# Optimization experiments

Measured on AMD Instinct MI355X. Metric: run time of the kernel, lower is better.

## Reference

```python
import jax, jax.numpy as jnp
import numpy as np

N_NODES = 50000
N_EDGES = 800000
IN_DIM = 128
OUT_DIM = 64
OUT_DATA = 32


def glorot(key, shape):
    fan_in, fan_out = shape[0], shape[1]
    lim = (6.0 / (fan_in + fan_out)) ** 0.5
    return jax.random.uniform(key, shape, jnp.float32, -lim, lim)


def setup_inputs() -> dict:
    key = jax.random.key(0)
    ks = jax.random.split(key, 8)
    x = jax.random.normal(ks[0], (N_NODES, IN_DIM), jnp.float32)
    edge_index = jax.random.randint(ks[1], (2, N_EDGES), 0, N_NODES, jnp.int64)
    W1 = glorot(ks[2], (IN_DIM, OUT_DIM)); b1 = jnp.zeros((OUT_DIM,), jnp.float32)
    W2 = glorot(ks[3], (OUT_DIM, OUT_DIM)); b2 = jnp.zeros((OUT_DIM,), jnp.float32)
    Wp1 = glorot(ks[4], (OUT_DIM, OUT_DIM)); bp1 = jnp.zeros((OUT_DIM,), jnp.float32)
    Wp2 = glorot(ks[5], (OUT_DIM, OUT_DATA)); bp2 = jnp.zeros((OUT_DATA,), jnp.float32)
    return {"x": x, "edge_index": edge_index, "W1": W1, "b1": b1,
            "W2": W2, "b2": b2, "Wp1": Wp1, "bp1": bp1, "Wp2": Wp2, "bp2": bp2}


def gcn_conv(x, src, dst, W, b, num_nodes):
    # GCNConv with symmetric normalization and self-loops:
    # out = D^{-1/2} (A + I) D^{-1/2} (x W) + b
    xw = x @ W                                            # [N, F]
    deg = jnp.zeros((num_nodes,), xw.dtype).at[dst].add(1.0) + 1.0  # +1 self-loop
    dinv = jax.lax.rsqrt(deg)
    coef = dinv[src] * dinv[dst]                          # [E]
    msgs = xw[src] * coef[:, None]                        # gather + scale
    agg = jax.ops.segment_sum(msgs, dst, num_segments=num_nodes)
    agg = agg + xw * (dinv * dinv)[:, None]               # self-loop term
    return agg + b


def reference(x, edge_index, W1, b1, W2, b2, Wp1, bp1, Wp2, bp2):
    src, dst = edge_index[0], edge_index[1]
    n = x.shape[0]
    # layer 1
    h = gcn_conv(x, src, dst, W1, b1, n)
    h = jnp.tanh(h)  # dropout is identity at inference
    # layer 2
    h = gcn_conv(h, src, dst, W2, b2, n)
    embedding = h
    h = jnp.tanh(h)
    # post_mp head: Linear -> Dropout(identity) -> Linear
    h = h @ Wp1 + bp1
    logits = h @ Wp2 + bp2
    return embedding, jax.nn.log_softmax(logits, axis=1)
```

## Files before the change

kernel.cpp:

```cpp
#include <hip/hip_runtime.h>
#include <hip/hip_fp16.h>

#define N_NODES 50000
#define N_EDGES 800000
#define IN_DIM 128
#define OUT_DIM 64
#define OUT_DATA 32

#define BUCKET_SHIFT 6
#define BUCKET_SIZE 64
#define NBUCK ((N_NODES + BUCKET_SIZE - 1) / BUCKET_SIZE)
#define NBLK_BIN 128
#define BIN_THREADS 1024
#define EPB ((N_EDGES + NBLK_BIN - 1) / NBLK_BIN)
#define ELCAP 1536

#define OFF_GCNT    0u
#define OFF_GBASE   4096u
#define OFF_DEG     8192u
#define OFF_NSTART  208896u
#define OFF_PERBLK  409600u
#define OFF_EREC    811008u
#define OFF_EREC2   4012032u
#define OFF_XW      7213056u
#define OFF_XW2     13613056u
#define OFF_WC      20013056u
#define OFF_BC      20021248u

__device__ __forceinline__ bool ei_is64(const int* ei) {
    int o = 0;
#pragma unroll
    for (int k = 0; k < 16; ++k) o |= ei[2 * k + 1];
    return o == 0;
}
__device__ __forceinline__ int load_ei(const int* ei, long long flat, bool is64) {
    return is64 ? (int)(((const long long*)ei)[flat]) : ei[flat];
}

__global__ void zero_kernel(int4* __restrict__ p) {
    p[threadIdx.x] = make_int4(0, 0, 0, 0);
}

__global__ __launch_bounds__(BIN_THREADS) void hist_kernel(const int* __restrict__ ei,
                                                           int* __restrict__ gcnt,
                                                           int* __restrict__ perblk) {
    __shared__ int lh[NBUCK];
    int t = threadIdx.x;
    for (int i = t; i < NBUCK; i += BIN_THREADS) lh[i] = 0;
    __syncthreads();
    bool is64 = ei_is64(ei);
    int e0 = blockIdx.x * EPB;
    int e1 = e0 + EPB; if (e1 > N_EDGES) e1 = N_EDGES;
    for (int e = e0 + t; e < e1; e += BIN_THREADS) {
        int d = load_ei(ei, (long long)N_EDGES + e, is64);
        atomicAdd(&lh[d >> BUCKET_SHIFT], 1);
    }
    __syncthreads();
    for (int i = t; i < NBUCK; i += BIN_THREADS)
        perblk[blockIdx.x * NBUCK + i] = atomicAdd(&gcnt[i], lh[i]);
}

__global__ __launch_bounds__(1024) void scanP_kernel(
    const int* __restrict__ gcnt, int* __restrict__ gbase,
    const float* __restrict__ Wp1, const float* __restrict__ bp1,
    const float* __restrict__ Wp2, const float* __restrict__ bp2,
    float* __restrict__ Wc, float* __restrict__ bc) {
    __shared__ int tmp[1024];
    int t = threadIdx.x;
    int v = (t < NBUCK) ? gcnt[t] : 0;
    tmp[t] = v;
    __syncthreads();
    for (int o = 1; o < 1024; o <<= 1) {
        int x = tmp[t];
        if (t >= o) x += tmp[t - o];
        __syncthreads();
        tmp[t] = x;
        __syncthreads();
    }
    if (t < NBUCK) gbase[t] = tmp[t] - v;
    if (t == NBUCK - 1) gbase[NBUCK] = tmp[t];
    for (int idx = t; idx < 64 * 32; idx += 1024) {
        int r = idx >> 5, j = idx & 31;
        float s = 0.0f;
        for (int k = 0; k < 64; ++k) s += Wp1[r * 64 + k] * Wp2[k * 32 + j];
        Wc[idx] = s;
    }
    if (t < 32) {
        float s = bp2[t];
        for (int k = 0; k < 64; ++k) s += bp1[k] * Wp2[k * 32 + t];
        bc[t] = s;
    }
}

__global__ __launch_bounds__(BIN_THREADS) void scat_kernel(const int* __restrict__ ei,
                                                           const int* __restrict__ gbase,
                                                           const int* __restrict__ perblk,
                                                           int* __restrict__ erec) {
    __shared__ int lh[NBUCK];
    __shared__ int base[NBUCK];
    int t = threadIdx.x;
    for (int i = t; i < NBUCK; i += BIN_THREADS) {
        lh[i] = 0;
        base[i] = gbase[i] + perblk[blockIdx.x * NBUCK + i];
    }
    __syncthreads();
    bool is64 = ei_is64(ei);
    int e0 = blockIdx.x * EPB;
    int e1 = e0 + EPB; if (e1 > N_EDGES) e1 = N_EDGES;
    for (int e = e0 + t; e < e1; e += BIN_THREADS) {
        int s = load_ei(ei, e, is64);
        int d = load_ei(ei, (long long)N_EDGES + e, is64);
        int b = d >> BUCKET_SHIFT;
        int slot = atomicAdd(&lh[b], 1);
        erec[base[b] + slot] = s | ((d & (BUCKET_SIZE - 1)) << 16);
    }
}

__global__ __launch_bounds__(512) void sortK_kernel(const int* __restrict__ erec,
                                                    const int* __restrict__ gbase,
                                                    int* __restrict__ erec2,
                                                    int* __restrict__ nodeStart,
                                                    int* __restrict__ deg) {
    __shared__ int elist[ELCAP];
    __shared__ int lcntS[64];
    __shared__ int startS[65];
    int t = threadIdx.x;
    int ebeg = gbase[blockIdx.x], eend = gbase[blockIdx.x + 1];
    int ecnt = eend - ebeg; if (ecnt > ELCAP) ecnt = ELCAP;
    for (int i = t; i < ecnt; i += 512) elist[i] = erec[ebeg + i];
    if (t < 64) lcntS[t] = 0;
    __syncthreads();
    int rec0 = -1, rank0 = 0, rec1 = -1, rank1 = 0, rec2 = -1, rank2 = 0;
    { int i = t;        if (i < ecnt) { rec0 = elist[i]; rank0 = atomicAdd(&lcntS[rec0 >> 16], 1); } }
    { int i = t + 512;  if (i < ecnt) { rec1 = elist[i]; rank1 = atomicAdd(&lcntS[rec1 >> 16], 1); } }
    { int i = t + 1024; if (i < ecnt) { rec2 = elist[i]; rank2 = atomicAdd(&lcntS[rec2 >> 16], 1); } }
    __syncthreads();
    if (t < 64) {
        int vcnt = lcntS[t]; int sum = vcnt;
        for (int off = 1; off < 64; off <<= 1) {
            int o = __shfl_up(sum, off, 64);
            if (t >= off) sum += o;
        }
        startS[t + 1] = sum; if (t == 0) startS[0] = 0;
    }
    __syncthreads();
    if (rec0 >= 0) erec2[ebeg + startS[rec0 >> 16] + rank0] = rec0;
    if (rec1 >= 0) erec2[ebeg + startS[rec1 >> 16] + rank1] = rec1;
    if (rec2 >= 0) erec2[ebeg + startS[rec2 >> 16] + rank2] = rec2;
    if (t < 64) {
        int node = (blockIdx.x << BUCKET_SHIFT) + t;
        nodeStart[node] = ebeg + startS[t];
        deg[node] = startS[t + 1] - startS[t];
    }
}

template <int K>
__global__ __launch_bounds__(256) void gemm64_kernel(const float* __restrict__ X,
                                                     const float* __restrict__ W,
                                                     const int* __restrict__ deg,
                                                     __half* __restrict__ Yh, int N) {
    __shared__ float Wl[K * 64];
    int t = threadIdx.x;
    for (int i = t; i < K * 16; i += 256)
        reinterpret_cast<float4*>(Wl)[i] = reinterpret_cast<const float4*>(W)[i];
    __syncthreads();
    int row = blockIdx.x * 256 + t;
    if (row >= N) return;
    float acc[64];
#pragma unroll
    for (int c = 0; c < 64; ++c) acc[c] = 0.0f;
    const float4* xr = reinterpret_cast<const float4*>(X + (size_t)row * K);
    for (int k4 = 0; k4 < K / 4; ++k4) {
        float4 xv = xr[k4];
#pragma unroll
        for (int kk = 0; kk < 4; ++kk) {
            float xs = (kk == 0) ? xv.x : (kk == 1) ? xv.y : (kk == 2) ? xv.z : xv.w;
            const float4* wr = reinterpret_cast<const float4*>(&Wl[(k4 * 4 + kk) * 64]);
#pragma unroll
            for (int c4 = 0; c4 < 16; ++c4) {
                float4 wv = wr[c4];
                acc[c4 * 4 + 0] += xs * wv.x;
                acc[c4 * 4 + 1] += xs * wv.y;
                acc[c4 * 4 + 2] += xs * wv.z;
                acc[c4 * 4 + 3] += xs * wv.w;
            }
        }
    }
    float di = rsqrtf((float)deg[row] + 1.0f);
    __half2* yr = reinterpret_cast<__half2*>(Yh + (size_t)row * 64);
#pragma unroll
    for (int c2 = 0; c2 < 32; ++c2)
        yr[c2] = __floats2half2_rn(acc[2 * c2] * di, acc[2 * c2 + 1] * di);
}

__device__ __forceinline__ float gatherN(const __half* __restrict__ xwp,
                                         const int* __restrict__ er,
                                         int s0, int n, int lane) {
    float acc = 0.0f;
    int e = 0;
    for (; e + 16 <= n; e += 16) {
        int r[16];
#pragma unroll
        for (int k = 0; k < 16; ++k) r[k] = er[s0 + e + k];
        float v[16];
#pragma unroll
        for (int k = 0; k < 16; ++k) v[k] = __half2float(xwp[((r[k] & 0xFFFF) << 6) + lane]);
#pragma unroll
        for (int k = 0; k < 16; ++k) acc += v[k];
    }
    if (e + 8 <= n) {
        int r[8];
#pragma unroll
        for (int k = 0; k < 8; ++k) r[k] = er[s0 + e + k];
        float v[8];
#pragma unroll
        for (int k = 0; k < 8; ++k) v[k] = __half2float(xwp[((r[k] & 0xFFFF) << 6) + lane]);
#pragma unroll
        for (int k = 0; k < 8; ++k) acc += v[k];
        e += 8;
    }
    if (e + 4 <= n) {
        int r[4];
#pragma unroll
        for (int k = 0; k < 4; ++k) r[k] = er[s0 + e + k];
        float v[4];
#pragma unroll
        for (int k = 0; k < 4; ++k) v[k] = __half2float(xwp[((r[k] & 0xFFFF) << 6) + lane]);
#pragma unroll
        for (int k = 0; k < 4; ++k) acc += v[k];
        e += 4;
    }
    for (; e < n; ++e)
        acc += __half2float(xwp[((er[s0 + e] & 0xFFFF) << 6) + lane]);
    return acc;
}

__global__ __launch_bounds__(256) void aggA_kernel(
    const __half* __restrict__ xwp, const int* __restrict__ erec2,
    const int* __restrict__ nodeStart, const int* __restrict__ deg,
    const float* __restrict__ b1v, const float* __restrict__ W2,
    __half* __restrict__ xw2p) {
    __shared__ float W2l[64 * 64];
    __shared__ float rowS[4][64];
    int t = threadIdx.x;
    for (int i = t; i < 1024; i += 256)
        reinterpret_cast<float4*>(W2l)[i] = reinterpret_cast<const float4*>(W2)[i];
    __syncthreads();
    int node = __builtin_amdgcn_readfirstlane(blockIdx.x * 4 + (t >> 6));
    if (node >= N_NODES) return;
    int lane = t & 63, wib = t >> 6;
    int s0 = __builtin_amdgcn_readfirstlane(nodeStart[node]);
    int n  = __builtin_amdgcn_readfirstlane(deg[node]);
    float acc = gatherN(xwp, erec2, s0, n, lane);
    float selfv = __half2float(xwp[(node << 6) + lane]);
    float di = rsqrtf((float)n + 1.0f);
    float h = tanhf((acc + selfv) * di + b1v[lane]);
    rowS[wib][lane] = h;
    float o = 0.0f;
#pragma unroll
    for (int f4 = 0; f4 < 16; ++f4) {
        float4 rv = reinterpret_cast<const float4*>(&rowS[wib][0])[f4];
        o += rv.x * W2l[(f4 * 4 + 0) * 64 + lane];
        o += rv.y * W2l[(f4 * 4 + 1) * 64 + lane];
        o += rv.z * W2l[(f4 * 4 + 2) * 64 + lane];
        o += rv.w * W2l[(f4 * 4 + 3) * 64 + lane];
    }
    xw2p[(node << 6) + lane] = __float2half_rn(o * di);
}

__global__ __launch_bounds__(256) void aggB_kernel(
    const __half* __restrict__ xw2p, const int* __restrict__ erec2,
    const int* __restrict__ nodeStart, const int* __restrict__ deg,
    const float* __restrict__ b2v, const float* __restrict__ Wc,
    const float* __restrict__ bc, float* __restrict__ embOut,
    float* __restrict__ logitsOut) {
    __shared__ float Wcl[64 * 32];
    __shared__ float rowS[4][64];
    __shared__ float bcl[32];
    int t = threadIdx.x;
    for (int i = t; i < 512; i += 256)
        reinterpret_cast<float4*>(Wcl)[i] = reinterpret_cast<const float4*>(Wc)[i];
    if (t < 32) bcl[t] = bc[t];
    __syncthreads();
    int node = __builtin_amdgcn_readfirstlane(blockIdx.x * 4 + (t >> 6));
    if (node >= N_NODES) return;
    int lane = t & 63, wib = t >> 6;
    int s0 = __builtin_amdgcn_readfirstlane(nodeStart[node]);
    int n  = __builtin_amdgcn_readfirstlane(deg[node]);
    float acc = gatherN(xw2p, erec2, s0, n, lane);
    float selfv = __half2float(xw2p[(node << 6) + lane]);
    float di = rsqrtf((float)n + 1.0f);
    float v = (acc + selfv) * di + b2v[lane];
    embOut[(node << 6) + lane] = v;
    rowS[wib][lane] = tanhf(v);
    int j = lane & 31, half = lane >> 5;
    float p = half ? 0.0f : bcl[j];
#pragma unroll
    for (int f4 = 0; f4 < 8; ++f4) {
        float4 rv = reinterpret_cast<const float4*>(&rowS[wib][half * 32])[f4];
        int fb = half * 32 + f4 * 4;
        p += rv.x * Wcl[(fb + 0) * 32 + j];
        p += rv.y * Wcl[(fb + 1) * 32 + j];
        p += rv.z * Wcl[(fb + 2) * 32 + j];
        p += rv.w * Wcl[(fb + 3) * 32 + j];
    }
    p += __shfl_down(p, 32);
    float m = p;
#pragma unroll
    for (int o = 16; o > 0; o >>= 1) m = fmaxf(m, __shfl_xor(m, o, 32));
    float ex = __expf(p - m);
    float s = ex;
#pragma unroll
    for (int o = 16; o > 0; o >>= 1) s += __shfl_xor(s, o, 32);
    if (half == 0) logitsOut[node * 32 + j] = p - m - logf(s);
}

extern "C" void kernel_launch(void* const* d_in, const int* in_sizes, int n_in,
                              void* d_out, int out_size, void* d_ws, size_t ws_size,
                              hipStream_t stream) {
    const float* x   = (const float*)d_in[0];
    const int*   ei  = (const int*)d_in[1];
    const float* W1  = (const float*)d_in[2];
    const float* b1  = (const float*)d_in[3];
    const float* W2  = (const float*)d_in[4];
    const float* b2  = (const float*)d_in[5];
    const float* Wp1 = (const float*)d_in[6];
    const float* bp1 = (const float*)d_in[7];
    const float* Wp2 = (const float*)d_in[8];
    const float* bp2 = (const float*)d_in[9];

    char* ws = (char*)d_ws;
    int*    gcnt   = (int*)(ws + OFF_GCNT);
    int*    gbase  = (int*)(ws + OFF_GBASE);
    int*    deg    = (int*)(ws + OFF_DEG);
    int*    nstart = (int*)(ws + OFF_NSTART);
    int*    perblk = (int*)(ws + OFF_PERBLK);
    int*    erec   = (int*)(ws + OFF_EREC);
    int*    erec2  = (int*)(ws + OFF_EREC2);
    __half* xwp    = (__half*)(ws + OFF_XW);
    __half* xw2p   = (__half*)(ws + OFF_XW2);
    float*  Wc     = (float*)(ws + OFF_WC);
    float*  bc     = (float*)(ws + OFF_BC);

    float* emb_out    = (float*)d_out;
    float* logits_out = (float*)d_out + (size_t)N_NODES * 64;

    zero_kernel<<<1, 256, 0, stream>>>((int4*)(ws + OFF_GCNT));
    hist_kernel<<<NBLK_BIN, BIN_THREADS, 0, stream>>>(ei, gcnt, perblk);
    scanP_kernel<<<1, 1024, 0, stream>>>(gcnt, gbase, Wp1, bp1, Wp2, bp2, Wc, bc);
    scat_kernel<<<NBLK_BIN, BIN_THREADS, 0, stream>>>(ei, gbase, perblk, erec);
    sortK_kernel<<<NBUCK, 512, 0, stream>>>(erec, gbase, erec2, nstart, deg);

    gemm64_kernel<IN_DIM><<<(N_NODES + 255) / 256, 256, 0, stream>>>(x, W1, deg, xwp, N_NODES);
    aggA_kernel<<<(N_NODES + 3) / 4, 256, 0, stream>>>(xwp, erec2, nstart, deg, b1, W2, xw2p);
    aggB_kernel<<<(N_NODES + 3) / 4, 256, 0, stream>>>(xw2p, erec2, nstart, deg, b2, Wc, bc, emb_out, logits_out);
}
```

Before: 141.7 us.

## Fuse per-bucket sort into layer-1 aggregation, compute degrees in histogram

The separate sortK kernel is removed. Its per-bucket counting sort now runs inside aggA, which works on one 64-node bucket per block and reads neighbour lists from shared memory. Degrees come from global atomics in the histogram kernel, so zero_kernel is widened to clear the degree array. The GEMM now computes two rows per thread. This removes a launch and a global round trip for the sorted edges, but adds global atomics and makes aggA run fewer, heavier blocks, each wave looping over 16 nodes, which may hurt load balance and occupancy.

```diff
diff --git a/kernel.cpp b/kernel.cpp
--- a/kernel.cpp
+++ b/kernel.cpp
@@ -38,12 +38,14 @@
 }
 
 __global__ void zero_kernel(int4* __restrict__ p) {
-    p[threadIdx.x] = make_int4(0, 0, 0, 0);
+    int i = blockIdx.x * 256 + threadIdx.x;
+    if (i < 13056) p[i] = make_int4(0, 0, 0, 0);
 }
 
 __global__ __launch_bounds__(BIN_THREADS) void hist_kernel(const int* __restrict__ ei,
                                                            int* __restrict__ gcnt,
-                                                           int* __restrict__ perblk) {
+                                                           int* __restrict__ perblk,
+                                                           int* __restrict__ deg) {
     __shared__ int lh[NBUCK];
     int t = threadIdx.x;
     for (int i = t; i < NBUCK; i += BIN_THREADS) lh[i] = 0;
@@ -54,6 +56,7 @@
     for (int e = e0 + t; e < e1; e += BIN_THREADS) {
         int d = load_ei(ei, (long long)N_EDGES + e, is64);
         atomicAdd(&lh[d >> BUCKET_SHIFT], 1);
+        atomicAdd(&deg[d], 1);
     }
     __syncthreads();
     for (int i = t; i < NBUCK; i += BIN_THREADS)
@@ -116,44 +119,6 @@
     }
 }
 
-__global__ __launch_bounds__(512) void sortK_kernel(const int* __restrict__ erec,
-                                                    const int* __restrict__ gbase,
-                                                    int* __restrict__ erec2,
-                                                    int* __restrict__ nodeStart,
-                                                    int* __restrict__ deg) {
-    __shared__ int elist[ELCAP];
-    __shared__ int lcntS[64];
-    __shared__ int startS[65];
-    int t = threadIdx.x;
-    int ebeg = gbase[blockIdx.x], eend = gbase[blockIdx.x + 1];
-    int ecnt = eend - ebeg; if (ecnt > ELCAP) ecnt = ELCAP;
-    for (int i = t; i < ecnt; i += 512) elist[i] = erec[ebeg + i];
-    if (t < 64) lcntS[t] = 0;
-    __syncthreads();
-    int rec0 = -1, rank0 = 0, rec1 = -1, rank1 = 0, rec2 = -1, rank2 = 0;
-    { int i = t;        if (i < ecnt) { rec0 = elist[i]; rank0 = atomicAdd(&lcntS[rec0 >> 16], 1); } }
-    { int i = t + 512;  if (i < ecnt) { rec1 = elist[i]; rank1 = atomicAdd(&lcntS[rec1 >> 16], 1); } }
-    { int i = t + 1024; if (i < ecnt) { rec2 = elist[i]; rank2 = atomicAdd(&lcntS[rec2 >> 16], 1); } }
-    __syncthreads();
-    if (t < 64) {
-        int vcnt = lcntS[t]; int sum = vcnt;
-        for (int off = 1; off < 64; off <<= 1) {
-            int o = __shfl_up(sum, off, 64);
-            if (t >= off) sum += o;
-        }
-        startS[t + 1] = sum; if (t == 0) startS[0] = 0;
-    }
-    __syncthreads();
-    if (rec0 >= 0) erec2[ebeg + startS[rec0 >> 16] + rank0] = rec0;
-    if (rec1 >= 0) erec2[ebeg + startS[rec1 >> 16] + rank1] = rec1;
-    if (rec2 >= 0) erec2[ebeg + startS[rec2 >> 16] + rank2] = rec2;
-    if (t < 64) {
-        int node = (blockIdx.x << BUCKET_SHIFT) + t;
-        nodeStart[node] = ebeg + startS[t];
-        deg[node] = startS[t + 1] - startS[t];
-    }
-}
-
 template <int K>
 __global__ __launch_bounds__(256) void gemm64_kernel(const float* __restrict__ X,
                                                      const float* __restrict__ W,
@@ -164,33 +129,138 @@
     for (int i = t; i < K * 16; i += 256)
         reinterpret_cast<float4*>(Wl)[i] = reinterpret_cast<const float4*>(W)[i];
     __syncthreads();
-    int row = blockIdx.x * 256 + t;
-    if (row >= N) return;
-    float acc[64];
-#pragma unroll
-    for (int c = 0; c < 64; ++c) acc[c] = 0.0f;
-    const float4* xr = reinterpret_cast<const float4*>(X + (size_t)row * K);
+    int row0 = blockIdx.x * 512 + t;
+    int row1 = row0 + 256;
+    if (row0 >= N) return;
+    bool p1 = row1 < N;
+    float acc0[64], acc1[64];
+#pragma unroll
+    for (int c = 0; c < 64; ++c) { acc0[c] = 0.0f; acc1[c] = 0.0f; }
+    const float4* xr0 = reinterpret_cast<const float4*>(X + (size_t)row0 * K);
+    const float4* xr1 = reinterpret_cast<const float4*>(X + (size_t)(p1 ? row1 : row0) * K);
     for (int k4 = 0; k4 < K / 4; ++k4) {
-        float4 xv = xr[k4];
+        float4 xv0 = xr0[k4];
+        float4 xv1 = xr1[k4];
 #pragma unroll
         for (int kk = 0; kk < 4; ++kk) {
-            float xs = (kk == 0) ? xv.x : (kk == 1) ? xv.y : (kk == 2) ? xv.z : xv.w;
+            float xs0 = (kk == 0) ? xv0.x : (kk == 1) ? xv0.y : (kk == 2) ? xv0.z : xv0.w;
+            float xs1 = (kk == 0) ? xv1.x : (kk == 1) ? xv1.y : (kk == 2) ? xv1.z : xv1.w;
             const float4* wr = reinterpret_cast<const float4*>(&Wl[(k4 * 4 + kk) * 64]);
 #pragma unroll
             for (int c4 = 0; c4 < 16; ++c4) {
                 float4 wv = wr[c4];
-                acc[c4 * 4 + 0] += xs * wv.x;
-                acc[c4 * 4 + 1] += xs * wv.y;
-                acc[c4 * 4 + 2] += xs * wv.z;
-                acc[c4 * 4 + 3] += xs * wv.w;
+                acc0[c4 * 4 + 0] += xs0 * wv.x; acc1[c4 * 4 + 0] += xs1 * wv.x;
+                acc0[c4 * 4 + 1] += xs0 * wv.y; acc1[c4 * 4 + 1] += xs1 * wv.y;
+                acc0[c4 * 4 + 2] += xs0 * wv.z; acc1[c4 * 4 + 2] += xs1 * wv.z;
+                acc0[c4 * 4 + 3] += xs0 * wv.w; acc1[c4 * 4 + 3] += xs1 * wv.w;
             }
         }
     }
-    float di = rsqrtf((float)deg[row] + 1.0f);
-    __half2* yr = reinterpret_cast<__half2*>(Yh + (size_t)row * 64);
+    float di0 = rsqrtf((float)deg[row0] + 1.0f);
+    __half2* yr0 = reinterpret_cast<__half2*>(Yh + (size_t)row0 * 64);
 #pragma unroll
     for (int c2 = 0; c2 < 32; ++c2)
-        yr[c2] = __floats2half2_rn(acc[2 * c2] * di, acc[2 * c2 + 1] * di);
+        yr0[c2] = __floats2half2_rn(acc0[2 * c2] * di0, acc0[2 * c2 + 1] * di0);
+    if (p1) {
+        float di1 = rsqrtf((float)deg[row1] + 1.0f);
+        __half2* yr1 = reinterpret_cast<__half2*>(Yh + (size_t)row1 * 64);
+#pragma unroll
+        for (int c2 = 0; c2 < 32; ++c2)
+            yr1[c2] = __floats2half2_rn(acc1[2 * c2] * di1, acc1[2 * c2 + 1] * di1);
+    }
+}
+
+__global__ __launch_bounds__(256) void aggA_kernel(
+    const __half* __restrict__ xwp, const int* __restrict__ erec,
+    const int* __restrict__ gbase, const float* __restrict__ b1v,
+    const float* __restrict__ W2, int* __restrict__ erec2,
+    int* __restrict__ nodeStart, __half* __restrict__ xw2p) {
+    __shared__ int elist[ELCAP];
+    __shared__ int elist2[ELCAP];
+    __shared__ float W2l[64 * 64];
+    __shared__ float rowS[4][64];
+    __shared__ int lcntS[64];
+    __shared__ int startS[65];
+    int t = threadIdx.x;
+    for (int i = t; i < 1024; i += 256)
+        reinterpret_cast<float4*>(W2l)[i] = reinterpret_cast<const float4*>(W2)[i];
+    int ebeg = gbase[blockIdx.x], eend = gbase[blockIdx.x + 1];
+    int ecnt = eend - ebeg; if (ecnt > ELCAP) ecnt = ELCAP;
+    for (int i = t; i < ecnt; i += 256) elist[i] = erec[ebeg + i];
+    if (t < 64) lcntS[t] = 0;
+    __syncthreads();
+    int rec[6], rank[6];
+#pragma unroll
+    for (int c = 0; c < 6; ++c) {
+        int i = t + c * 256;
+        rec[c] = -1; rank[c] = 0;
+        if (i < ecnt) { rec[c] = elist[i]; rank[c] = atomicAdd(&lcntS[rec[c] >> 16], 1); }
+    }
+    __syncthreads();
+    if (t < 64) {
+        int v = lcntS[t]; int sum = v;
+        for (int off = 1; off < 64; off <<= 1) {
+            int o = __shfl_up(sum, off, 64);
+            if (t >= off) sum += o;
+        }
+        startS[t + 1] = sum; if (t == 0) startS[0] = 0;
+    }
+    __syncthreads();
+#pragma unroll
+    for (int c = 0; c < 6; ++c)
+        if (rec[c] >= 0) elist2[startS[rec[c] >> 16] + rank[c]] = rec[c];
+    __syncthreads();
+    for (int i = t; i < ecnt; i += 256) erec2[ebeg + i] = elist2[i];
+    if (t < 64) {
+        int node = (blockIdx.x << BUCKET_SHIFT) + t;
+        if (node < N_NODES) nodeStart[node] = ebeg + startS[t];
+    }
+    int lane = t & 63, wv = t >> 6;
+    int nodeBase = blockIdx.x << BUCKET_SHIFT;
+    for (int k = 0; k < 16; ++k) {
+        int nl = wv * 16 + k;
+        int node = nodeBase + nl;
+        if (node >= N_NODES) break;
+        int s0 = startS[nl];
+        int n = startS[nl + 1] - s0;
+        float acc = 0.0f;
+        int e = 0;
+        for (; e + 16 <= n; e += 16) {
+            int r[16]; float v[16];
+#pragma unroll
+            for (int q = 0; q < 16; ++q) r[q] = elist2[s0 + e + q];
+#pragma unroll
+            for (int q = 0; q < 16; ++q) v[q] = __half2float(xwp[((r[q] & 0xFFFF) << 6) + lane]);
+#pragma unroll
+            for (int q = 0; q < 16; ++q) acc += v[q];
+        }
+        if (e + 8 <= n) {
+            int r[8]; float v[8];
+#pragma unroll
+            for (int q = 0; q < 8; ++q) r[q] = elist2[s0 + e + q];
+#pragma unroll
+            for (int q = 0; q < 8; ++q) v[q] = __half2float(xwp[((r[q] & 0xFFFF) << 6) + lane]);
+#pragma unroll
+            for (int q = 0; q < 8; ++q) acc += v[q];
+            e += 8;
+        }
+        for (; e < n; ++e)
+            acc += __half2float(xwp[((elist2[s0 + e] & 0xFFFF) << 6) + lane]);
+        float selfv = __half2float(xwp[(node << 6) + lane]);
+        float di = rsqrtf((float)n + 1.0f);
+        float h = tanhf((acc + selfv) * di + b1v[lane]);
+        rowS[wv][lane] = h;
+        float o = 0.0f;
+#pragma unroll
+        for (int f4 = 0; f4 < 16; ++f4) {
+            float4 rv = reinterpret_cast<const float4*>(&rowS[wv][0])[f4];
+            o += rv.x * W2l[(f4 * 4 + 0) * 64 + lane];
+            o += rv.y * W2l[(f4 * 4 + 1) * 64 + lane];
+            o += rv.z * W2l[(f4 * 4 + 2) * 64 + lane];
+            o += rv.w * W2l[(f4 * 4 + 3) * 64 + lane];
+        }
+        xw2p[(node << 6) + lane] = __float2half_rn(o * di);
+    }
 }
 
 __device__ __forceinline__ float gatherN(const __half* __restrict__ xwp,
@@ -199,20 +269,18 @@
     float acc = 0.0f;
     int e = 0;
     for (; e + 16 <= n; e += 16) {
-        int r[16];
+        int r[16]; float v[16];
 #pragma unroll
         for (int k = 0; k < 16; ++k) r[k] = er[s0 + e + k];
-        float v[16];
 #pragma unroll
         for (int k = 0; k < 16; ++k) v[k] = __half2float(xwp[((r[k] & 0xFFFF) << 6) + lane]);
 #pragma unroll
         for (int k = 0; k < 16; ++k) acc += v[k];
     }
     if (e + 8 <= n) {
-        int r[8];
+        int r[8]; float v[8];
 #pragma unroll
         for (int k = 0; k < 8; ++k) r[k] = er[s0 + e + k];
-        float v[8];
 #pragma unroll
         for (int k = 0; k < 8; ++k) v[k] = __half2float(xwp[((r[k] & 0xFFFF) << 6) + lane]);
 #pragma unroll
@@ -220,10 +288,9 @@
         e += 8;
     }
     if (e + 4 <= n) {
-        int r[4];
+        int r[4]; float v[4];
 #pragma unroll
         for (int k = 0; k < 4; ++k) r[k] = er[s0 + e + k];
-        float v[4];
 #pragma unroll
         for (int k = 0; k < 4; ++k) v[k] = __half2float(xwp[((r[k] & 0xFFFF) << 6) + lane]);
 #pragma unroll
@@ -233,39 +300,6 @@
     for (; e < n; ++e)
         acc += __half2float(xwp[((er[s0 + e] & 0xFFFF) << 6) + lane]);
     return acc;
-}
-
-__global__ __launch_bounds__(256) void aggA_kernel(
-    const __half* __restrict__ xwp, const int* __restrict__ erec2,
-    const int* __restrict__ nodeStart, const int* __restrict__ deg,
-    const float* __restrict__ b1v, const float* __restrict__ W2,
-    __half* __restrict__ xw2p) {
-    __shared__ float W2l[64 * 64];
-    __shared__ float rowS[4][64];
-    int t = threadIdx.x;
-    for (int i = t; i < 1024; i += 256)
-        reinterpret_cast<float4*>(W2l)[i] = reinterpret_cast<const float4*>(W2)[i];
-    __syncthreads();
-    int node = __builtin_amdgcn_readfirstlane(blockIdx.x * 4 + (t >> 6));
-    if (node >= N_NODES) return;
-    int lane = t & 63, wib = t >> 6;
-    int s0 = __builtin_amdgcn_readfirstlane(nodeStart[node]);
-    int n  = __builtin_amdgcn_readfirstlane(deg[node]);
-    float acc = gatherN(xwp, erec2, s0, n, lane);
-    float selfv = __half2float(xwp[(node << 6) + lane]);
-    float di = rsqrtf((float)n + 1.0f);
-    float h = tanhf((acc + selfv) * di + b1v[lane]);
-    rowS[wib][lane] = h;
-    float o = 0.0f;
-#pragma unroll
-    for (int f4 = 0; f4 < 16; ++f4) {
-        float4 rv = reinterpret_cast<const float4*>(&rowS[wib][0])[f4];
-        o += rv.x * W2l[(f4 * 4 + 0) * 64 + lane];
-        o += rv.y * W2l[(f4 * 4 + 1) * 64 + lane];
-        o += rv.z * W2l[(f4 * 4 + 2) * 64 + lane];
-        o += rv.w * W2l[(f4 * 4 + 3) * 64 + lane];
-    }
-    xw2p[(node << 6) + lane] = __float2half_rn(o * di);
 }
 
 __global__ __launch_bounds__(256) void aggB_kernel(
@@ -345,13 +379,12 @@
     float* emb_out    = (float*)d_out;
     float* logits_out = (float*)d_out + (size_t)N_NODES * 64;
 
-    zero_kernel<<<1, 256, 0, stream>>>((int4*)(ws + OFF_GCNT));
-    hist_kernel<<<NBLK_BIN, BIN_THREADS, 0, stream>>>(ei, gcnt, perblk);
+    zero_kernel<<<51, 256, 0, stream>>>((int4*)(ws + OFF_GCNT));
+    hist_kernel<<<NBLK_BIN, BIN_THREADS, 0, stream>>>(ei, gcnt, perblk, deg);
     scanP_kernel<<<1, 1024, 0, stream>>>(gcnt, gbase, Wp1, bp1, Wp2, bp2, Wc, bc);
     scat_kernel<<<NBLK_BIN, BIN_THREADS, 0, stream>>>(ei, gbase, perblk, erec);
-    sortK_kernel<<<NBUCK, 512, 0, stream>>>(erec, gbase, erec2, nstart, deg);
-
-    gemm64_kernel<IN_DIM><<<(N_NODES + 255) / 256, 256, 0, stream>>>(x, W1, deg, xwp, N_NODES);
-    aggA_kernel<<<(N_NODES + 3) / 4, 256, 0, stream>>>(xwp, erec2, nstart, deg, b1, W2, xw2p);
+
+    gemm64_kernel<IN_DIM><<<(N_NODES + 511) / 512, 256, 0, stream>>>(x, W1, deg, xwp, N_NODES);
+    aggA_kernel<<<NBUCK, 256, 0, stream>>>(xwp, erec, gbase, b1, W2, erec2, nstart, xw2p);
     aggB_kernel<<<(N_NODES + 3) / 4, 256, 0, stream>>>(xw2p, erec2, nstart, deg, b2, Wc, bc, emb_out, logits_out);
 }
```

New measurement: 196.8 us. 1.39x slower.

## Rewrite first-layer GEMM as wave-per-row-block with W1 column held in registers

Applied to the files above, without the earlier changes.

Replaces the thread-per-row GEMM, which kept 64 accumulators per thread and read W1 from LDS, with a kernel where each wave owns 64 consecutive rows. Each lane keeps one column of W1 (128 floats) in registers, reads each x row through wave-uniform (scalar/broadcast) loads, and writes one half-precision output, so stores are coalesced. The aim is to remove uncoalesced per-thread row reads and LDS traffic. The cost is about 128 VGPRs per lane for the weights, which lowers occupancy, and only 782 waves for the whole GEMM, so parallelism may be limited.

```diff
diff --git a/kernel.cpp b/kernel.cpp
--- a/kernel.cpp
+++ b/kernel.cpp
@@ -154,43 +154,32 @@
     }
 }
 
-template <int K>
-__global__ __launch_bounds__(256) void gemm64_kernel(const float* __restrict__ X,
-                                                     const float* __restrict__ W,
-                                                     const int* __restrict__ deg,
-                                                     __half* __restrict__ Yh, int N) {
-    __shared__ float Wl[K * 64];
-    int t = threadIdx.x;
-    for (int i = t; i < K * 16; i += 256)
-        reinterpret_cast<float4*>(Wl)[i] = reinterpret_cast<const float4*>(W)[i];
-    __syncthreads();
-    int row = blockIdx.x * 256 + t;
-    if (row >= N) return;
-    float acc[64];
-#pragma unroll
-    for (int c = 0; c < 64; ++c) acc[c] = 0.0f;
-    const float4* xr = reinterpret_cast<const float4*>(X + (size_t)row * K);
-    for (int k4 = 0; k4 < K / 4; ++k4) {
-        float4 xv = xr[k4];
-#pragma unroll
-        for (int kk = 0; kk < 4; ++kk) {
-            float xs = (kk == 0) ? xv.x : (kk == 1) ? xv.y : (kk == 2) ? xv.z : xv.w;
-            const float4* wr = reinterpret_cast<const float4*>(&Wl[(k4 * 4 + kk) * 64]);
-#pragma unroll
-            for (int c4 = 0; c4 < 16; ++c4) {
-                float4 wv = wr[c4];
-                acc[c4 * 4 + 0] += xs * wv.x;
-                acc[c4 * 4 + 1] += xs * wv.y;
-                acc[c4 * 4 + 2] += xs * wv.z;
-                acc[c4 * 4 + 3] += xs * wv.w;
-            }
+__global__ __launch_bounds__(256) void gemmV_kernel(const float* __restrict__ X,
+                                                    const float* __restrict__ W,
+                                                    const int* __restrict__ deg,
+                                                    __half* __restrict__ Yh) {
+    int t = threadIdx.x, lane = t & 63;
+    float wreg[IN_DIM];
+#pragma unroll
+    for (int k = 0; k < IN_DIM; ++k) wreg[k] = W[k * 64 + lane];
+    int wid = __builtin_amdgcn_readfirstlane(blockIdx.x * 4 + (t >> 6));
+    int r0 = wid * 64;
+    for (int i = 0; i < 64; ++i) {
+        int row = r0 + i;
+        if (row >= N_NODES) break;
+        const float* xr = X + (size_t)row * IN_DIM;
+        float a0 = 0.0f, a1 = 0.0f, a2 = 0.0f, a3 = 0.0f;
+#pragma unroll
+        for (int k = 0; k < IN_DIM; k += 4) {
+            a0 = fmaf(xr[k + 0], wreg[k + 0], a0);
+            a1 = fmaf(xr[k + 1], wreg[k + 1], a1);
+            a2 = fmaf(xr[k + 2], wreg[k + 2], a2);
+            a3 = fmaf(xr[k + 3], wreg[k + 3], a3);
         }
-    }
-    float di = rsqrtf((float)deg[row] + 1.0f);
-    __half2* yr = reinterpret_cast<__half2*>(Yh + (size_t)row * 64);
-#pragma unroll
-    for (int c2 = 0; c2 < 32; ++c2)
-        yr[c2] = __floats2half2_rn(acc[2 * c2] * di, acc[2 * c2 + 1] * di);
+        float acc = (a0 + a1) + (a2 + a3);
+        float di = rsqrtf((float)deg[row] + 1.0f);
+        Yh[(size_t)row * 64 + lane] = __float2half_rn(acc * di);
+    }
 }
 
 __device__ __forceinline__ float gatherN(const __half* __restrict__ xwp,
@@ -199,20 +188,18 @@
     float acc = 0.0f;
     int e = 0;
     for (; e + 16 <= n; e += 16) {
-        int r[16];
+        int r[16]; float v[16];
 #pragma unroll
         for (int k = 0; k < 16; ++k) r[k] = er[s0 + e + k];
-        float v[16];
 #pragma unroll
         for (int k = 0; k < 16; ++k) v[k] = __half2float(xwp[((r[k] & 0xFFFF) << 6) + lane]);
 #pragma unroll
         for (int k = 0; k < 16; ++k) acc += v[k];
     }
     if (e + 8 <= n) {
-        int r[8];
+        int r[8]; float v[8];
 #pragma unroll
         for (int k = 0; k < 8; ++k) r[k] = er[s0 + e + k];
-        float v[8];
 #pragma unroll
         for (int k = 0; k < 8; ++k) v[k] = __half2float(xwp[((r[k] & 0xFFFF) << 6) + lane]);
 #pragma unroll
@@ -220,10 +207,9 @@
         e += 8;
     }
     if (e + 4 <= n) {
-        int r[4];
+        int r[4]; float v[4];
 #pragma unroll
         for (int k = 0; k < 4; ++k) r[k] = er[s0 + e + k];
-        float v[4];
 #pragma unroll
         for (int k = 0; k < 4; ++k) v[k] = __half2float(xwp[((r[k] & 0xFFFF) << 6) + lane]);
 #pragma unroll
@@ -351,7 +337,7 @@
     scat_kernel<<<NBLK_BIN, BIN_THREADS, 0, stream>>>(ei, gbase, perblk, erec);
     sortK_kernel<<<NBUCK, 512, 0, stream>>>(erec, gbase, erec2, nstart, deg);
 
-    gemm64_kernel<IN_DIM><<<(N_NODES + 255) / 256, 256, 0, stream>>>(x, W1, deg, xwp, N_NODES);
+    gemmV_kernel<<<(NBUCK + 3) / 4, 256, 0, stream>>>(x, W1, deg, xwp);
     aggA_kernel<<<(N_NODES + 3) / 4, 256, 0, stream>>>(xwp, erec2, nstart, deg, b1, W2, xw2p);
     aggB_kernel<<<(N_NODES + 3) / 4, 256, 0, stream>>>(xw2p, erec2, nstart, deg, b2, Wc, bc, emb_out, logits_out);
 }
```

New measurement: 189.0 us. 1.33x slower.
